# Performance work log

Hardware: AMD Instinct MI355X
Metric: run time of the kernel (lower is better)

Reference implementation:

```python
import jax, jax.numpy as jnp
import numpy as np

N_STATE = 1024
N_HEAD = 16
B, S = 2, 2048
NEG = -1e9  # finite stand-in for -inf in the additive causal mask


def setup_inputs() -> dict:
    key = jax.random.key(0)
    ks = jax.random.split(key, 8)
    sd = N_STATE ** -0.5
    x = jax.random.normal(ks[0], (B, S, N_STATE), dtype=jnp.float32)
    # additive causal mask, as in Whisper: upper triangle = -inf
    i = jnp.arange(S)
    mask = jnp.where(i[None, :] > i[:, None], NEG, 0.0).astype(jnp.float32)
    return {
        "x": x,
        "mask": mask,
        "Wq": jax.random.normal(ks[1], (N_STATE, N_STATE), jnp.float32) * sd,
        "bq": jax.random.normal(ks[2], (N_STATE,), jnp.float32) * 0.02,
        "Wk": jax.random.normal(ks[3], (N_STATE, N_STATE), jnp.float32) * sd,
        "Wv": jax.random.normal(ks[4], (N_STATE, N_STATE), jnp.float32) * sd,
        "bv": jax.random.normal(ks[5], (N_STATE,), jnp.float32) * 0.02,
        "Wo": jax.random.normal(ks[6], (N_STATE, N_STATE), jnp.float32) * sd,
        "bo": jax.random.normal(ks[7], (N_STATE,), jnp.float32) * 0.02,
    }


def reference(x, mask, Wq, bq, Wk, Wv, bv, Wo, bo):
    B_, S_, D = x.shape
    H = N_HEAD
    hd = D // H
    scale = hd ** -0.25  # applied to both q and k, per the source

    q = (x @ Wq + bq).reshape(B_, S_, H, hd) * scale   # [B,S,H,hd]
    k = (x @ Wk).reshape(B_, S_, H, hd) * scale        # key has no bias
    v = (x @ Wv + bv).reshape(B_, S_, H, hd)

    qk = jnp.einsum("bqhd,bkhd->bhqk", q, k) + mask[:S_, :S_]
    w = jax.nn.softmax(qk.astype(jnp.float32), axis=-1).astype(q.dtype)
    o = jnp.einsum("bhqk,bkhd->bqhd", w, v).reshape(B_, S_, D)
    return o @ Wo + bo
```

## Files before the change

### kernel.cpp

```cpp
#include <hip/hip_runtime.h>
#include <hip/hip_bf16.h>

#define BB 2
#define SS 2048
#define DD 1024
#define HH 16
#define HD 64
#define QKSCALE 0.35355339059327373f
#define QKSCALE_E2 0.42466090144f
#define NEGBIG (-1e9f)

using u16 = unsigned short;
typedef __attribute__((ext_vector_type(8))) short short8;
typedef __attribute__((ext_vector_type(4))) float floatx4;
typedef __attribute__((ext_vector_type(4))) unsigned short ushort4v;

#define GLOBAL_AS __attribute__((address_space(1)))
#define LDS_AS __attribute__((address_space(3)))

__device__ __forceinline__ u16 f2b(float f) {
  union { float f; unsigned u; } v; v.f = f;
  return (u16)((v.u + 0x7fffu + ((v.u >> 16) & 1u)) >> 16);
}

__device__ __forceinline__ u16 bconv(float f) {
  union { __hip_bfloat16 h; u16 u; } cv;
  cv.h = __float2bfloat16(f);
  return cv.u;
}

__device__ __forceinline__ float ex2(float f) {
  return __builtin_amdgcn_exp2f(f);
}

__device__ __forceinline__ floatx4 vmax4(floatx4 a, floatx4 b) {
  return (floatx4){fmaxf(a[0], b[0]), fmaxf(a[1], b[1]),
                   fmaxf(a[2], b[2]), fmaxf(a[3], b[3])};
}

__device__ __forceinline__ void gload_lds16(const void* g, void* l) {
  __builtin_amdgcn_global_load_lds((GLOBAL_AS void*)(g), (LDS_AS void*)(l), 16, 0, 0);
}

__global__ __launch_bounds__(256) void cvt_bf16x4(const float4* __restrict__ src,
                                                  ushort4v* __restrict__ dst, int n4) {
  int i = blockIdx.x * 256 + threadIdx.x;
  if (i >= n4) return;
  float4 f = src[i];
  ushort4v o = { f2b(f.x), f2b(f.y), f2b(f.z), f2b(f.w) };
  dst[i] = o;
}

__global__ __launch_bounds__(256) void transpose_w(const float* __restrict__ s0,
                                                   const float* __restrict__ s1,
                                                   const float* __restrict__ s2,
                                                   const float* __restrict__ s3,
                                                   u16* __restrict__ dst) {
  __shared__ float tile[32][33];
  const float* src = (blockIdx.z == 0) ? s0 : (blockIdx.z == 1) ? s1
                   : (blockIdx.z == 2) ? s2 : s3;
  u16* d = dst + (size_t)blockIdx.z * 1024 * 1024;
  int c0 = blockIdx.x * 32, r0 = blockIdx.y * 32;
  int tx = threadIdx.x, ty = threadIdx.y;
#pragma unroll
  for (int i = 0; i < 4; ++i)
    tile[ty + i * 8][tx] = src[(size_t)(r0 + ty + i * 8) * 1024 + c0 + tx];
  __syncthreads();
#pragma unroll
  for (int i = 0; i < 4; ++i)
    d[(size_t)(c0 + ty + i * 8) * 1024 + r0 + tx] = f2b(tile[tx][ty + i * 8]);
}

__global__ __launch_bounds__(256) void transpose_v(const u16* __restrict__ v,
                                                   u16* __restrict__ vtd) {
  __shared__ u16 tile[32][34];
  int b = blockIdx.z;
  int c0 = blockIdx.x * 32;
  int s0 = blockIdx.y * 32;
  int tx = threadIdx.x, ty = threadIdx.y;
#pragma unroll
  for (int i = 0; i < 4; ++i)
    tile[ty + i * 8][tx] = v[(size_t)(b * SS + s0 + ty + i * 8) * DD + c0 + tx];
  __syncthreads();
#pragma unroll
  for (int i = 0; i < 4; ++i)
    vtd[(size_t)(b * DD + c0 + ty + i * 8) * SS + s0 + tx] = tile[tx][ty + i * 8];
}

template <typename OutT>
__global__ __launch_bounds__(256, 3)
void gemm_bt(const u16* __restrict__ A, const u16* __restrict__ Bt,
             OutT* __restrict__ C, const float* __restrict__ bias,
             float scale, int M, int N, int K) {
  const int tid = threadIdx.x;
  const int lane = tid & 63;
  const int w = tid >> 6;
  const int m0 = blockIdx.x * 64;
  const int n0 = blockIdx.y * 128;
  __shared__ u16 As[2][64 * 64];
  __shared__ u16 Bs[2][128 * 64];
  floatx4 acc[2][4];
#pragma unroll
  for (int i = 0; i < 2; ++i)
#pragma unroll
    for (int j = 0; j < 4; ++j) acc[i][j] = (floatx4){0.f, 0.f, 0.f, 0.f};

  const int wr = (w >> 1) * 32;
  const int wc = (w & 1) * 64;
  const int g = lane >> 4;
  const int lr = lane & 15;
  const size_t strideA = (size_t)K * 2;

  auto stage = [&](int k0, int buf) {
#pragma unroll
    for (int p = 0; p < 2; ++p) {
      int L = tid * 16 + p * 4096;
      int row = L >> 7;
      int cb = (L ^ ((row & 7) << 4)) & 127;
      gload_lds16((const char*)A + (size_t)(m0 + row) * strideA + k0 * 2 + cb,
                  (char*)As[buf] + p * 4096 + w * 1024);
    }
#pragma unroll
    for (int p = 0; p < 4; ++p) {
      int L = tid * 16 + p * 4096;
      int row = L >> 7;
      int cb = (L ^ ((row & 7) << 4)) & 127;
      gload_lds16((const char*)Bt + (size_t)(n0 + row) * strideA + k0 * 2 + cb,
                  (char*)Bs[buf] + p * 4096 + w * 1024);
    }
  };

  const int nsteps = K >> 6;
  stage(0, 0);
  for (int t = 0; t < nsteps; ++t) {
    const int buf = t & 1;
    __syncthreads();
    if (t + 1 < nsteps) stage((t + 1) << 6, buf ^ 1);
    const u16* as = As[buf];
    const u16* bs = Bs[buf];
#pragma unroll
    for (int ks = 0; ks < 2; ++ks) {
      short8 af[2], bf[4];
      const int c0 = ks * 32 + g * 8;
#pragma unroll
      for (int mi = 0; mi < 2; ++mi) {
        int row = wr + mi * 16 + lr;
        af[mi] = *(const short8*)(as + row * 64 + (c0 ^ ((row & 7) << 3)));
      }
#pragma unroll
      for (int ni = 0; ni < 4; ++ni) {
        int row = wc + ni * 16 + lr;
        bf[ni] = *(const short8*)(bs + row * 64 + (c0 ^ ((row & 7) << 3)));
      }
      __builtin_amdgcn_s_setprio(1);
#pragma unroll
      for (int mi = 0; mi < 2; ++mi)
#pragma unroll
        for (int ni = 0; ni < 4; ++ni)
          acc[mi][ni] = __builtin_amdgcn_mfma_f32_16x16x32_bf16(af[mi], bf[ni],
                                                                acc[mi][ni], 0, 0, 0);
      __builtin_amdgcn_s_setprio(0);
    }
  }
#pragma unroll
  for (int ni = 0; ni < 4; ++ni) {
    int col = n0 + wc + ni * 16 + lr;
    float bvv = bias ? bias[col] : 0.f;
#pragma unroll
    for (int mi = 0; mi < 2; ++mi) {
#pragma unroll
      for (int r = 0; r < 4; ++r) {
        int rowg = m0 + wr + mi * 16 + g * 4 + r;
        float val = (acc[mi][ni][r] + bvv) * scale;
        if constexpr (sizeof(OutT) == 4) C[(size_t)rowg * N + col] = val;
        else C[(size_t)rowg * N + col] = (OutT)f2b(val);
      }
    }
  }
}

__global__ __launch_bounds__(256, 4)
void gemm_qkv(const u16* __restrict__ A, const u16* __restrict__ Wt3,
              u16* __restrict__ Out3, const float* __restrict__ bq,
              const float* __restrict__ bv) {
  const int seg = blockIdx.z;
  const u16* Bt = Wt3 + (size_t)seg * 1024 * 1024;
  u16* C = Out3 + (size_t)seg * 4096 * 1024;
  const float* bias = (seg == 0) ? bq : (seg == 2) ? bv : nullptr;
  const float scale = (seg == 2) ? 1.0f : QKSCALE_E2;

  const int tid = threadIdx.x;
  const int lane = tid & 63;
  const int w = tid >> 6;
  const int m0 = blockIdx.x * 128;
  const int n0 = blockIdx.y * 128;
  __shared__ u16 As[2][64 * 64];
  __shared__ u16 Bs[2][64 * 64];
  floatx4 acc[4][4];
#pragma unroll
  for (int i = 0; i < 4; ++i)
#pragma unroll
    for (int j = 0; j < 4; ++j) acc[i][j] = (floatx4){0.f, 0.f, 0.f, 0.f};
  const int wr = (w >> 1) * 64;
  const int wc = (w & 1) * 64;
  const int g = lane >> 4;
  const int lr = lane & 15;

  auto stage = [&](int k0, int buf) {
#pragma unroll
    for (int p = 0; p < 2; ++p) {
      int L = tid * 16 + p * 4096;
      int lrow = L >> 7;
      int un = (L & 127) ^ ((lrow & 7) << 4);
      int r = lrow * 2 + (un >> 6);
      int cb = un & 63;
      gload_lds16((const char*)A + (size_t)(m0 + r) * 2048 + k0 * 2 + cb,
                  (char*)As[buf] + p * 4096 + w * 1024);
      gload_lds16((const char*)Bt + (size_t)(n0 + r) * 2048 + k0 * 2 + cb,
                  (char*)Bs[buf] + p * 4096 + w * 1024);
    }
  };

  stage(0, 0);
  for (int t = 0; t < 32; ++t) {
    const int buf = t & 1;
    __syncthreads();
    if (t + 1 < 32) stage((t + 1) << 5, buf ^ 1);
    const u16* as = As[buf];
    const u16* bs = Bs[buf];
    short8 af[4], bf[4];
#pragma unroll
    for (int mi = 0; mi < 4; ++mi) {
      int r = wr + mi * 16 + lr;
      af[mi] = *(const short8*)((const char*)as +
               ((r >> 1) * 128 + ((((r & 1) << 6) | (g * 16)) ^ (((r >> 1) & 7) << 4))));
    }
#pragma unroll
    for (int ni = 0; ni < 4; ++ni) {
      int r = wc + ni * 16 + lr;
      bf[ni] = *(const short8*)((const char*)bs +
               ((r >> 1) * 128 + ((((r & 1) << 6) | (g * 16)) ^ (((r >> 1) & 7) << 4))));
    }
    __builtin_amdgcn_s_setprio(1);
#pragma unroll
    for (int mi = 0; mi < 4; ++mi)
#pragma unroll
      for (int ni = 0; ni < 4; ++ni)
        acc[mi][ni] = __builtin_amdgcn_mfma_f32_16x16x32_bf16(af[mi], bf[ni],
                                                              acc[mi][ni], 0, 0, 0);
    __builtin_amdgcn_s_setprio(0);
  }
#pragma unroll
  for (int ni = 0; ni < 4; ++ni) {
    int col = n0 + wc + ni * 16 + lr;
    float bvv = bias ? bias[col] : 0.f;
#pragma unroll
    for (int mi = 0; mi < 4; ++mi) {
#pragma unroll
      for (int r = 0; r < 4; ++r) {
        int rowg = m0 + wr + mi * 16 + g * 4 + r;
        C[(size_t)rowg * 1024 + col] = f2b((acc[mi][ni][r] + bvv) * scale);
      }
    }
  }
}

__device__ __forceinline__ void stream_softmax(floatx4 (&sa)[4], float& m, float& l,
                                               floatx4 (&acc)[4], u16* pl,
                                               bool diag, int wlr, int g, int lr) {
  if (diag) {
#pragma unroll
    for (int ct = 0; ct < 4; ++ct)
#pragma unroll
      for (int r = 0; r < 4; ++r)
        if (ct * 16 + g * 4 + r > wlr) sa[ct][r] += NEGBIG;
  }
  floatx4 v = vmax4(vmax4(sa[0], sa[1]), vmax4(sa[2], sa[3]));
  float mx = fmaxf(fmaxf(v[0], v[1]), fmaxf(v[2], v[3]));
  mx = fmaxf(mx, __shfl_xor(mx, 16, 64));
  mx = fmaxf(mx, __shfl_xor(mx, 32, 64));
  if (!__all(mx <= m + 8.f)) {
    float mn = fmaxf(m, mx);
    float al = ex2(m - mn);
    l *= al;
#pragma unroll
    for (int dt = 0; dt < 4; ++dt) acc[dt] *= al;
    m = mn;
  }
  floatx4 p[4];
#pragma unroll
  for (int ct = 0; ct < 4; ++ct)
#pragma unroll
    for (int r = 0; r < 4; ++r)
      p[ct][r] = ex2(sa[ct][r] - m);
  floatx4 s = (p[0] + p[1]) + (p[2] + p[3]);
  float rs = (s[0] + s[1]) + (s[2] + s[3]);
  rs += __shfl_xor(rs, 16, 64);
  rs += __shfl_xor(rs, 32, 64);
  l += rs;
#pragma unroll
  for (int ct = 0; ct < 4; ++ct) {
    ushort4v pk = { bconv(p[ct][0]), bconv(p[ct][1]),
                    bconv(p[ct][2]), bconv(p[ct][3]) };
    *(ushort4v*)((char*)pl + ((lr * 128 + ct * 32 + g * 8) ^ ((lr & 7) << 4))) = pk;
  }
}

__global__ __launch_bounds__(256, 4)
void flash_attn(const u16* __restrict__ q, const u16* __restrict__ k,
                const u16* __restrict__ vt, u16* __restrict__ o) {
  const int tid = threadIdx.x;
  const int lane = tid & 63;
  const int w = tid >> 6;
  const int g = lane >> 4;
  const int lr = lane & 15;
  const int i = (int)blockIdx.x;
  const int x = i & 7;
  const int kk = i >> 3;
  const int s = kk & 3;
  const int mI = kk >> 2;
  const int u = mI >> 3;
  const int v = mI & 7;
  const int gg = x * 4 + s;
  const int b = gg >> 4;
  const int h = gg & 15;
  const int a = (u + s) & 3;
  const int qt = (a == 0) ? v : (a == 1) ? (31 - v) : (a == 2) ? (16 + v) : (15 - v);
  const int row0 = qt * 64 + w * 16;
  const int wlr = w * 16 + lr;

  __shared__ u16 Ks[2][64 * 64];
  __shared__ u16 Vs[2][64 * 64];
  __shared__ u16 Pl[4][16 * 64];

  short8 qf[2];
  {
    const u16* qp = q + (size_t)(b * SS + row0 + lr) * DD + h * HD + g * 8;
    qf[0] = *(const short8*)qp;
    qf[1] = *(const short8*)(qp + 32);
  }
  floatx4 acc[4];
#pragma unroll
  for (int dt = 0; dt < 4; ++dt) acc[dt] = (floatx4){0.f, 0.f, 0.f, 0.f};
  float m = -1e30f, l = 0.f;

  const char* kbase = (const char*)(k + (size_t)(b * SS) * DD + h * HD);
  const char* vbase = (const char*)(vt + (size_t)((b * HH + h) * HD) * SS);
  const int nt = qt + 1;

  auto stage = [&](int t, int buf) {
    const int kvb = t * 64;
#pragma unroll
    for (int p = 0; p < 2; ++p) {
      int L = tid * 16 + p * 4096;
      int row = L >> 7;
      int cb = (L ^ ((row & 7) << 4)) & 127;
      gload_lds16(kbase + (size_t)(kvb + row) * (DD * 2) + cb,
                  (char*)Ks + buf * 8192 + p * 4096 + w * 1024);
      gload_lds16(vbase + (size_t)row * (SS * 2) + kvb * 2 + cb,
                  (char*)Vs + buf * 8192 + p * 4096 + w * 1024);
    }
  };

  stage(0, 0);
  int cur = 0;
  for (int t = 0; t < nt; ++t) {
    __syncthreads();
    if (t + 1 < nt) stage(t + 1, cur ^ 1);
    const u16* kc = Ks[cur];
    const u16* vc = Vs[cur];

    floatx4 sa[4];
#pragma unroll
    for (int ct = 0; ct < 4; ++ct) sa[ct] = (floatx4){0.f, 0.f, 0.f, 0.f};
    __builtin_amdgcn_s_setprio(1);
#pragma unroll
    for (int ks = 0; ks < 2; ++ks) {
      const int c0 = ks * 32 + g * 8;
#pragma unroll
      for (int ct = 0; ct < 4; ++ct) {
        int row = ct * 16 + lr;
        short8 kf = *(const short8*)(kc + row * 64 + (c0 ^ ((row & 7) << 3)));
        sa[ct] = __builtin_amdgcn_mfma_f32_16x16x32_bf16(kf, qf[ks], sa[ct], 0, 0, 0);
      }
    }
    __builtin_amdgcn_s_setprio(0);

    stream_softmax(sa, m, l, acc, Pl[w], t == qt, wlr, g, lr);

    __builtin_amdgcn_s_setprio(1);
#pragma unroll
    for (int ks = 0; ks < 2; ++ks) {
      const int c0 = ks * 32 + g * 8;
      int pby = (lr * 128 + ks * 64 + g * 16) ^ ((lr & 7) << 4);
      short8 pf = *(const short8*)((const char*)Pl[w] + pby);
#pragma unroll
      for (int dt = 0; dt < 4; ++dt) {
        int row = dt * 16 + lr;
        short8 vf = *(const short8*)(vc + row * 64 + (c0 ^ ((row & 7) << 3)));
        acc[dt] = __builtin_amdgcn_mfma_f32_16x16x32_bf16(vf, pf, acc[dt], 0, 0, 0);
      }
    }
    __builtin_amdgcn_s_setprio(0);
    cur ^= 1;
  }

  float inv = 1.0f / l;
#pragma unroll
  for (int dt = 0; dt < 4; ++dt) {
    ushort4v pa = { bconv(acc[dt][0] * inv), bconv(acc[dt][1] * inv),
                    bconv(acc[dt][2] * inv), bconv(acc[dt][3] * inv) };
    *(ushort4v*)(o + (size_t)(b * SS + row0 + lr) * DD + h * HD + dt * 16 + g * 4) = pa;
  }
}

extern "C" void kernel_launch(void* const* d_in, const int* in_sizes, int n_in,
                              void* d_out, int out_size, void* d_ws, size_t ws_size,
                              hipStream_t stream) {
  const float* x  = (const float*)d_in[0];
  const float* Wq = (const float*)d_in[2];
  const float* bq = (const float*)d_in[3];
  const float* Wk = (const float*)d_in[4];
  const float* Wv = (const float*)d_in[5];
  const float* bv = (const float*)d_in[6];
  const float* Wo = (const float*)d_in[7];
  const float* bo = (const float*)d_in[8];
  float* out = (float*)d_out;

  char* ws = (char*)d_ws;
  u16* xb  = (u16*)(ws);
  u16* wt  = (u16*)(ws + (8u << 20));
  u16* qkv = (u16*)(ws + (16u << 20));
  u16* vb  = qkv + 2u * 4096 * 1024;
  u16* vtb = (u16*)(ws + (40u << 20));
  u16* ob  = (u16*)(ws + (48u << 20));
  u16* wot = wt + 3u * 1024 * 1024;

  dim3 tb(32, 8);
  cvt_bf16x4<<<4096, 256, 0, stream>>>((const float4*)x, (ushort4v*)xb,
                                       (BB * SS * DD) / 4);
  transpose_w<<<dim3(32, 32, 4), tb, 0, stream>>>(Wq, Wk, Wv, Wo, wt);
  gemm_qkv<<<dim3(32, 8, 3), 256, 0, stream>>>(xb, wt, qkv, bq, bv);
  transpose_v<<<dim3(32, 64, 2), tb, 0, stream>>>(vb, vtb);
  flash_attn<<<1024, 256, 0, stream>>>(qkv, qkv + (size_t)4096 * 1024, vtb, ob);
  gemm_bt<float><<<dim3(64, 8), 256, 0, stream>>>(ob, wot, out, bo, 1.0f,
                                                  4096, 1024, 1024);
}
```

Measured before the change: 112.8 us.

## Use 128-row query bands per 512-thread block sharing staged K/V tiles

The flash attention kernel now processes 128 query rows per block using 8 waves instead of 64 rows with 4 waves. Each staged K/V tile is shared by twice as many waves, which halves the global-to-LDS traffic per query row. The block-to-tile mapping is simplified to pair heavy and light causal bands. In exchange, the lower waves in each band sit idle on the final tile past their diagonal, and the grid has half as many blocks, giving coarser load balance.

```diff
diff --git a/kernel.cpp b/kernel.cpp
--- a/kernel.cpp
+++ b/kernel.cpp
@@ -306,7 +306,7 @@
   }
 }
 
-__global__ __launch_bounds__(256, 4)
+__global__ __launch_bounds__(512, 2)
 void flash_attn(const u16* __restrict__ q, const u16* __restrict__ k,
                 const u16* __restrict__ vt, u16* __restrict__ o) {
   const int tid = threadIdx.x;
@@ -314,24 +314,22 @@
   const int w = tid >> 6;
   const int g = lane >> 4;
   const int lr = lane & 15;
-  const int i = (int)blockIdx.x;
-  const int x = i & 7;
-  const int kk = i >> 3;
-  const int s = kk & 3;
-  const int mI = kk >> 2;
-  const int u = mI >> 3;
-  const int v = mI & 7;
-  const int gg = x * 4 + s;
-  const int b = gg >> 4;
-  const int h = gg & 15;
-  const int a = (u + s) & 3;
-  const int qt = (a == 0) ? v : (a == 1) ? (31 - v) : (a == 2) ? (16 + v) : (15 - v);
-  const int row0 = qt * 64 + w * 16;
-  const int wlr = w * 16 + lr;
+  const int id = (int)blockIdx.x;
+  const int x = id & 7;
+  const int s = (id >> 3) & 15;
+  const int head = x * 4 + (id >> 7);
+  const int b = head >> 4;
+  const int h = head & 15;
+  const int kq = s >> 1;
+  const int band = (s & 1) ? kq : 15 - kq;
+  const int row0 = band * 128 + w * 16;
+  const int wlr = (w & 3) * 16 + lr;
+  const int diagT = 2 * band + (w >> 2);
+  const int nt = 2 * band + 2;
 
   __shared__ u16 Ks[2][64 * 64];
   __shared__ u16 Vs[2][64 * 64];
-  __shared__ u16 Pl[4][16 * 64];
+  __shared__ u16 Pl[8][16 * 64];
 
   short8 qf[2];
   {
@@ -346,20 +344,15 @@
 
   const char* kbase = (const char*)(k + (size_t)(b * SS) * DD + h * HD);
   const char* vbase = (const char*)(vt + (size_t)((b * HH + h) * HD) * SS);
-  const int nt = qt + 1;
 
   auto stage = [&](int t, int buf) {
-    const int kvb = t * 64;
-#pragma unroll
-    for (int p = 0; p < 2; ++p) {
-      int L = tid * 16 + p * 4096;
-      int row = L >> 7;
-      int cb = (L ^ ((row & 7) << 4)) & 127;
-      gload_lds16(kbase + (size_t)(kvb + row) * (DD * 2) + cb,
-                  (char*)Ks + buf * 8192 + p * 4096 + w * 1024);
-      gload_lds16(vbase + (size_t)row * (SS * 2) + kvb * 2 + cb,
-                  (char*)Vs + buf * 8192 + p * 4096 + w * 1024);
-    }
+    int L = tid * 16;
+    int row = L >> 7;
+    int cb = (L ^ ((row & 7) << 4)) & 127;
+    gload_lds16(kbase + (size_t)(t * 64 + row) * (DD * 2) + cb,
+                (char*)Ks[buf] + w * 1024);
+    gload_lds16(vbase + (size_t)row * (SS * 2) + t * 128 + cb,
+                (char*)Vs[buf] + w * 1024);
   };
 
   stage(0, 0);
@@ -367,41 +360,43 @@
   for (int t = 0; t < nt; ++t) {
     __syncthreads();
     if (t + 1 < nt) stage(t + 1, cur ^ 1);
-    const u16* kc = Ks[cur];
-    const u16* vc = Vs[cur];
-
-    floatx4 sa[4];
-#pragma unroll
-    for (int ct = 0; ct < 4; ++ct) sa[ct] = (floatx4){0.f, 0.f, 0.f, 0.f};
-    __builtin_amdgcn_s_setprio(1);
-#pragma unroll
-    for (int ks = 0; ks < 2; ++ks) {
-      const int c0 = ks * 32 + g * 8;
-#pragma unroll
-      for (int ct = 0; ct < 4; ++ct) {
-        int row = ct * 16 + lr;
-        short8 kf = *(const short8*)(kc + row * 64 + (c0 ^ ((row & 7) << 3)));
-        sa[ct] = __builtin_amdgcn_mfma_f32_16x16x32_bf16(kf, qf[ks], sa[ct], 0, 0, 0);
-      }
-    }
-    __builtin_amdgcn_s_setprio(0);
-
-    stream_softmax(sa, m, l, acc, Pl[w], t == qt, wlr, g, lr);
-
-    __builtin_amdgcn_s_setprio(1);
-#pragma unroll
-    for (int ks = 0; ks < 2; ++ks) {
-      const int c0 = ks * 32 + g * 8;
-      int pby = (lr * 128 + ks * 64 + g * 16) ^ ((lr & 7) << 4);
-      short8 pf = *(const short8*)((const char*)Pl[w] + pby);
-#pragma unroll
-      for (int dt = 0; dt < 4; ++dt) {
-        int row = dt * 16 + lr;
-        short8 vf = *(const short8*)(vc + row * 64 + (c0 ^ ((row & 7) << 3)));
-        acc[dt] = __builtin_amdgcn_mfma_f32_16x16x32_bf16(vf, pf, acc[dt], 0, 0, 0);
-      }
-    }
-    __builtin_amdgcn_s_setprio(0);
+    if (t <= diagT) {
+      const u16* kc = Ks[cur];
+      const u16* vc = Vs[cur];
+
+      floatx4 sa[4];
+#pragma unroll
+      for (int ct = 0; ct < 4; ++ct) sa[ct] = (floatx4){0.f, 0.f, 0.f, 0.f};
+      __builtin_amdgcn_s_setprio(1);
+#pragma unroll
+      for (int ks = 0; ks < 2; ++ks) {
+        const int c0 = ks * 32 + g * 8;
+#pragma unroll
+        for (int ct = 0; ct < 4; ++ct) {
+          int row = ct * 16 + lr;
+          short8 kf = *(const short8*)(kc + row * 64 + (c0 ^ ((row & 7) << 3)));
+          sa[ct] = __builtin_amdgcn_mfma_f32_16x16x32_bf16(kf, qf[ks], sa[ct], 0, 0, 0);
+        }
+      }
+      __builtin_amdgcn_s_setprio(0);
+
+      stream_softmax(sa, m, l, acc, Pl[w], t == diagT, wlr, g, lr);
+
+      __builtin_amdgcn_s_setprio(1);
+#pragma unroll
+      for (int ks = 0; ks < 2; ++ks) {
+        const int c0 = ks * 32 + g * 8;
+        int pby = (lr * 128 + ks * 64 + g * 16) ^ ((lr & 7) << 4);
+        short8 pf = *(const short8*)((const char*)Pl[w] + pby);
+#pragma unroll
+        for (int dt = 0; dt < 4; ++dt) {
+          int row = dt * 16 + lr;
+          short8 vf = *(const short8*)(vc + row * 64 + (c0 ^ ((row & 7) << 3)));
+          acc[dt] = __builtin_amdgcn_mfma_f32_16x16x32_bf16(vf, pf, acc[dt], 0, 0, 0);
+        }
+      }
+      __builtin_amdgcn_s_setprio(0);
+    }
     cur ^= 1;
   }
 
@@ -442,7 +437,7 @@
   transpose_w<<<dim3(32, 32, 4), tb, 0, stream>>>(Wq, Wk, Wv, Wo, wt);
   gemm_qkv<<<dim3(32, 8, 3), 256, 0, stream>>>(xb, wt, qkv, bq, bv);
   transpose_v<<<dim3(32, 64, 2), tb, 0, stream>>>(vb, vtb);
-  flash_attn<<<1024, 256, 0, stream>>>(qkv, qkv + (size_t)4096 * 1024, vtb, ob);
+  flash_attn<<<512, 512, 0, stream>>>(qkv, qkv + (size_t)4096 * 1024, vtb, ob);
   gemm_bt<float><<<dim3(64, 8), 256, 0, stream>>>(ob, wot, out, bo, 1.0f,
                                                   4096, 1024, 1024);
 }
```

Measured after the change: 124.6 us. 1.1x slower.
